# Optimization experiments

Measured on AMD Instinct MI355X. Metric: run time of the kernel, lower is better.

## Reference

```python
import jax, jax.numpy as jnp
import numpy as np

B, S, E = 8, 2048, 1024

def setup_inputs() -> dict:
    key = jax.random.key(0)
    ks = jax.random.split(key, 7)
    scale = 1.0 / np.sqrt(E)
    return {
        "x": jax.random.normal(ks[0], (B, S, E), dtype=jnp.float32),
        "Wq": jax.random.normal(ks[1], (E, E), dtype=jnp.float32) * scale,
        "bq": jax.random.normal(ks[2], (E,), dtype=jnp.float32) * 0.01,
        "Wk": jax.random.normal(ks[3], (E, E), dtype=jnp.float32) * scale,
        "bk": jax.random.normal(ks[4], (E,), dtype=jnp.float32) * 0.01,
        "Wv": jax.random.normal(ks[5], (E, E), dtype=jnp.float32) * scale,
        "bv": jax.random.normal(ks[6], (E,), dtype=jnp.float32) * 0.01,
    }

def reference(x, Wq, bq, Wk, bk, Wv, bv):
    # torch Linear: y = x @ W^T + b
    q = jnp.einsum('bse,fe->bsf', x, Wq) + bq  # [B,S,E]
    k = jnp.einsum('bse,fe->bsf', x, Wk) + bk
    v = jnp.einsum('bse,fe->bsf', x, Wv) + bv
    # unscaled, unmasked single-head attention (faithful to source)
    scores = jnp.einsum('bqe,bke->bqk', q, k)  # [B,S,S]
    attn = jax.nn.softmax(scores, axis=-1)
    return jnp.einsum('bqk,bke->bqe', attn, v)  # [B,S,E]
```

## Files before the change

kernel.cpp:

```cpp
#include <hip/hip_runtime.h>
#include <math.h>

typedef _Float16 f16;
typedef _Float16 f16x8 __attribute__((ext_vector_type(8)));
typedef _Float16 f16x4 __attribute__((ext_vector_type(4)));
typedef float f32x4v __attribute__((ext_vector_type(4)));

#define Bb 8
#define Ss 2048
#define Ee 1024
#define BSr (Bb*Ss)
#define MB 1048576ull

__device__ __forceinline__ void gll16(const void* gp, void* lp) {
    __builtin_amdgcn_global_load_lds(
        (const __attribute__((address_space(1))) unsigned int*)gp,
        (__attribute__((address_space(3))) unsigned int*)lp,
        16, 0, 0);
}

#define MFMA16(a, b, c) __builtin_amdgcn_mfma_f32_16x16x32_f16((a), (b), (c), 0, 0, 0)
#define SBAR() asm volatile("s_barrier" ::: "memory")

__global__ __launch_bounds__(256)
void split_xw(const float* __restrict__ x, const float* __restrict__ Wv,
              f16* __restrict__ xh, f16* __restrict__ Wvh)
{
    const int bid = blockIdx.x;
    const float* src; f16* dst; int i;
    if (bid < 16384) { src = x;  dst = xh;  i = (bid * 256 + threadIdx.x) * 4; }
    else             { src = Wv; dst = Wvh; i = ((bid - 16384) * 256 + threadIdx.x) * 4; }
    float4 v = *(const float4*)&src[i];
    f16x4 h4;
    h4[0] = (f16)v.x; h4[1] = (f16)v.y; h4[2] = (f16)v.z; h4[3] = (f16)v.w;
    *(f16x4*)&dst[i] = h4;
}

__global__ __launch_bounds__(256)
void transpose_split(const float* __restrict__ Wq, const float* __restrict__ Wk,
                     f16* __restrict__ WqTh, f16* __restrict__ WqTl,
                     f16* __restrict__ WkTh, f16* __restrict__ WkTl)
{
    __shared__ float ts[64][65];
    const int z = blockIdx.z;
    const float* W = z ? Wk : Wq;
    f16* Th = z ? WkTh : WqTh;
    f16* Tl = z ? WkTl : WqTl;
    const int e0 = blockIdx.x * 64, j0 = blockIdx.y * 64;
    const int t = threadIdx.x;
    {
        const int jj = t >> 2, c0 = (t & 3) * 16;
        #pragma unroll
        for (int m = 0; m < 4; ++m) {
            float4 v = *(const float4*)&W[(size_t)(j0 + jj) * Ee + e0 + c0 + m * 4];
            ts[jj][c0 + m*4 + 0] = v.x; ts[jj][c0 + m*4 + 1] = v.y;
            ts[jj][c0 + m*4 + 2] = v.z; ts[jj][c0 + m*4 + 3] = v.w;
        }
    }
    __syncthreads();
    {
        const int ee = t >> 2, jc0 = (t & 3) * 16;
        f16x8 h0, h1, l0, l1;
        #pragma unroll
        for (int m = 0; m < 16; ++m) {
            float val = ts[jc0 + m][ee];
            f16 hh = (f16)val; f16 ll = (f16)(val - (float)hh);
            if (m < 8) { h0[m] = hh; l0[m] = ll; }
            else       { h1[m-8] = hh; l1[m-8] = ll; }
        }
        size_t off = (size_t)(e0 + ee) * Ee + j0 + jc0;
        *(f16x8*)&Th[off]     = h0; *(f16x8*)&Th[off + 8] = h1;
        *(f16x8*)&Tl[off]     = l0; *(f16x8*)&Tl[off + 8] = l1;
    }
}

__global__ __launch_bounds__(256)
void compute_Mt(const f16* __restrict__ WkTh, const f16* __restrict__ WkTl,
                const f16* __restrict__ WqTh, const f16* __restrict__ WqTl,
                float* __restrict__ Mpart)
{
    __shared__ f16 Ah[128][32];
    __shared__ f16 Al[128][32];
    __shared__ f16 Bh[128][32];
    __shared__ f16 Bl[128][32];

    const int bn = blockIdx.x, bm = blockIdx.y, z = blockIdx.z;
    const int t = threadIdx.x;
    const int lane = t & 63;
    const int w = t >> 6;
    const int wr = w >> 1, wc = w & 1;
    const int lr = lane & 15;
    const int kq = (lane >> 4) << 3;
    const int rS = w * 32 + (lane >> 2);
    const int eS = (lane & 3) * 8;

    const f16* gAh = WkTh + ((size_t)(bm * 128 + rS)) * Ee + z * 256 + eS;
    const f16* gAl = WkTl + ((size_t)(bm * 128 + rS)) * Ee + z * 256 + eS;
    const f16* gBh = WqTh + ((size_t)(bn * 128 + rS)) * Ee + z * 256 + eS;
    const f16* gBl = WqTl + ((size_t)(bn * 128 + rS)) * Ee + z * 256 + eS;

    f32x4v acc[4][4];
    #pragma unroll
    for (int i = 0; i < 4; ++i)
        #pragma unroll
        for (int j = 0; j < 4; ++j) acc[i][j] = (f32x4v)0.f;

    for (int k0 = 0; k0 < 256; k0 += 32) {
        __syncthreads();
        #pragma unroll
        for (int c = 0; c < 2; ++c) {
            const size_t go = (size_t)c * 16 * Ee + k0;
            const int lo = w * 1024 + c * 512;
            gll16(gAh + go, &Ah[0][0] + lo);
            gll16(gAl + go, &Al[0][0] + lo);
            gll16(gBh + go, &Bh[0][0] + lo);
            gll16(gBl + go, &Bl[0][0] + lo);
        }
        __syncthreads();

        f16x8 fah[4], fal[4], fbh[4], fbl[4];
        #pragma unroll
        for (int i = 0; i < 4; ++i) {
            fah[i] = *(const f16x8*)&Ah[wr * 64 + i * 16 + lr][kq];
            fal[i] = *(const f16x8*)&Al[wr * 64 + i * 16 + lr][kq];
            fbh[i] = *(const f16x8*)&Bh[wc * 64 + i * 16 + lr][kq];
            fbl[i] = *(const f16x8*)&Bl[wc * 64 + i * 16 + lr][kq];
        }
        #pragma unroll
        for (int i = 0; i < 4; ++i)
            #pragma unroll
            for (int j = 0; j < 4; ++j) {
                acc[i][j] = MFMA16(fah[i], fbh[j], acc[i][j]);
                acc[i][j] = MFMA16(fah[i], fbl[j], acc[i][j]);
                acc[i][j] = MFMA16(fal[i], fbh[j], acc[i][j]);
            }
    }

    #pragma unroll
    for (int i = 0; i < 4; ++i) {
        #pragma unroll
        for (int j = 0; j < 4; ++j) {
            const int col = bn * 128 + wc * 64 + j * 16 + lr;
            #pragma unroll
            for (int r = 0; r < 4; ++r) {
                const int row = bm * 128 + wr * 64 + i * 16 + (lane >> 4) * 4 + r;
                Mpart[(size_t)z * MB + (size_t)row * Ee + col] = acc[i][j][r];
            }
        }
    }
}

__global__ __launch_bounds__(256)
void reduce_Mt(const float* __restrict__ Mpart, f16* __restrict__ Mth, f16* __restrict__ Mtl)
{
    const size_t i4 = ((size_t)blockIdx.x * 256 + threadIdx.x) * 4;
    float4 a = *(const float4*)&Mpart[i4];
    float4 b = *(const float4*)&Mpart[MB + i4];
    float4 c = *(const float4*)&Mpart[2 * MB + i4];
    float4 d = *(const float4*)&Mpart[3 * MB + i4];
    float s[4] = {a.x + b.x + c.x + d.x, a.y + b.y + c.y + d.y,
                  a.z + b.z + c.z + d.z, a.w + b.w + c.w + d.w};
    f16x4 h, l;
    #pragma unroll
    for (int m = 0; m < 4; ++m) { f16 hh = (f16)s[m]; h[m] = hh; l[m] = (f16)(s[m] - (float)hh); }
    *(f16x4*)&Mth[i4] = h;
    *(f16x4*)&Mtl[i4] = l;
}

__global__ __launch_bounds__(256)
void wker(const float* __restrict__ Wk, const float* __restrict__ bq,
          float* __restrict__ wpart)
{
    const int f = (blockIdx.x & 3) * 256 + threadIdx.x;
    const int p = blockIdx.x >> 2;
    float acc = 0.f;
    for (int j = p * 128; j < p * 128 + 128; ++j)
        acc += Wk[(size_t)j * Ee + f] * bq[j];
    wpart[p * Ee + f] = acc;
}

__global__ __launch_bounds__(256)
void vker(const f16* __restrict__ xh, const float* __restrict__ wpart,
          float* __restrict__ vbuf)
{
    __shared__ float wsum[1024];
    const int t = threadIdx.x;
    for (int ff = t; ff < 1024; ff += 256) {
        float s = 0.f;
        #pragma unroll
        for (int p = 0; p < 8; ++p) s += wpart[p * Ee + ff];
        wsum[ff] = s;
    }
    __syncthreads();
    const int lane = t & 63;
    const int row = blockIdx.x * 4 + (t >> 6);
    const f16* xr = xh + (size_t)row * Ee + lane * 16;
    f16x8 a = *(const f16x8*)&xr[0];
    f16x8 b = *(const f16x8*)&xr[8];
    float acc = 0.f;
    #pragma unroll
    for (int m = 0; m < 8; ++m) {
        acc += (float)a[m] * wsum[lane * 16 + m];
        acc += (float)b[m] * wsum[lane * 16 + 8 + m];
    }
    #pragma unroll
    for (int off = 1; off < 64; off <<= 1) acc += __shfl_xor(acc, off, 64);
    if (lane == 0) vbuf[row] = acc;
}

template<bool DUAL>
__device__ __forceinline__ void kloop32(
    const f16* __restrict__ Ag, const int sA,
    const f16* __restrict__ Bhg, const f16* __restrict__ Blg, const int sB,
    const int NT, f16* __restrict__ lds,
    f32x4v acc[8][4], const int w, const int lane)
{
    constexpr int SETF = DUAL ? 24576 : 16384;
    const int wr = w >> 2, wc = w & 3;
    const int srcA = (w * 16 + (lane & 15)) * sA + (lane >> 4) * 8;
    const int srcB = (w * 16 + (lane & 15)) * sB + (lane >> 4) * 8;
    const int lrd = lane * 8;

#define STAGE8(t, s) do {                                                   \
        const int k0_ = (t) * 32;                                           \
        const f16* gA_ = Ag + k0_ + srcA;                                   \
        const f16* gB_ = Bhg + k0_ + srcB;                                  \
        f16* dA_ = lds + (s) * SETF + w * 512;                              \
        f16* dB_ = lds + (s) * SETF + 8192 + w * 512;                       \
        gll16(gA_,                       dA_);                              \
        gll16(gA_ + (size_t)8 * 16 * sA, dA_ + 8 * 512);                    \
        gll16(gB_,                       dB_);                              \
        gll16(gB_ + (size_t)8 * 16 * sB, dB_ + 8 * 512);                    \
        if (DUAL) {                                                         \
            const f16* gL_ = Blg + k0_ + srcB;                              \
            f16* dL_ = lds + (s) * SETF + 16384 + w * 512;                  \
            gll16(gL_,                       dL_);                          \
            gll16(gL_ + (size_t)8 * 16 * sB, dL_ + 8 * 512);                \
        }                                                                   \
    } while (0)

    STAGE8(0, 0);
    STAGE8(1, 1);
    if (DUAL) asm volatile("s_waitcnt vmcnt(6)" ::: "memory");
    else      asm volatile("s_waitcnt vmcnt(4)" ::: "memory");
    SBAR();

    for (int t = 0; t < NT; ++t) {
        const int s = t % 3;
        if (t + 2 < NT) STAGE8(t + 2, (t + 2) % 3);

        const f16* As = lds + s * SETF;
        const f16* Bh = As + 8192;
        const f16* Bl = As + 16384;
        f16x8 fa[8], fbh[4], fbl[4];
        #pragma unroll
        for (int i = 0; i < 8; ++i)
            fa[i] = *(const f16x8*)(As + (wr * 8 + i) * 512 + lrd);
        #pragma unroll
        for (int j = 0; j < 4; ++j)
            fbh[j] = *(const f16x8*)(Bh + (wc * 4 + j) * 512 + lrd);
        if (DUAL) {
            #pragma unroll
            for (int j = 0; j < 4; ++j)
                fbl[j] = *(const f16x8*)(Bl + (wc * 4 + j) * 512 + lrd);
        }
        #pragma unroll
        for (int j = 0; j < 4; ++j)
            #pragma unroll
            for (int i = 0; i < 8; ++i) {
                acc[i][j] = MFMA16(fa[i], fbh[j], acc[i][j]);
                if (DUAL)
                    acc[i][j] = MFMA16(fa[i], fbl[j], acc[i][j]);
            }

        if (t + 2 < NT) {
            if (DUAL) asm volatile("s_waitcnt vmcnt(6)" ::: "memory");
            else      asm volatile("s_waitcnt vmcnt(4)" ::: "memory");
        } else if (t + 1 < NT) {
            asm volatile("s_waitcnt vmcnt(0)" ::: "memory");
        }
        SBAR();
    }
#undef STAGE8
}

__global__ __launch_bounds__(512, 2)
void proj3(const f16* __restrict__ xh,
           const f16* __restrict__ Mth, const f16* __restrict__ Mtl,
           const f16* __restrict__ Wvh, const float* __restrict__ bv,
           f16* __restrict__ qp, f16* __restrict__ vT)
{
    __shared__ f16 lds[73728];

    const int lin = blockIdx.x;
    const int l = (lin & 7) * 64 + (lin >> 3);
    const int zc = l & 7;
    const int by = l >> 3;
    const int z = zc >> 2;
    const int col0 = (zc & 3) * 256;
    const int row0 = by * 256;

    const int t = threadIdx.x;
    const int lane = t & 63;
    const int w = t >> 6;
    const int wr = w >> 2, wc = w & 3;

    f32x4v acc[8][4];
    #pragma unroll
    for (int i = 0; i < 8; ++i)
        #pragma unroll
        for (int j = 0; j < 4; ++j) acc[i][j] = (f32x4v)0.f;

    const f16* Ax = xh + (size_t)row0 * Ee;
    if (z == 0) {
        kloop32<true>(Ax, Ee, Mth + (size_t)col0 * Ee, Mtl + (size_t)col0 * Ee, Ee,
                      32, lds, acc, w, lane);
        #pragma unroll
        for (int i = 0; i < 8; ++i) {
            #pragma unroll
            for (int j = 0; j < 4; ++j) {
                const int col = col0 + wc * 64 + j * 16 + (lane & 15);
                #pragma unroll
                for (int r = 0; r < 4; ++r) {
                    const int row = row0 + wr * 128 + i * 16 + (lane >> 4) * 4 + r;
                    qp[(size_t)row * Ee + col] = (f16)acc[i][j][r];
                }
            }
        }
    } else {
        kloop32<false>(Ax, Ee, Wvh + (size_t)col0 * Ee, Wvh + (size_t)col0 * Ee, Ee,
                       32, lds, acc, w, lane);
        #pragma unroll
        for (int i = 0; i < 8; ++i) {
            #pragma unroll
            for (int j = 0; j < 4; ++j) {
                const int e = col0 + wc * 64 + j * 16 + (lane & 15);
                const float b = bv[e];
                const int srow = row0 + wr * 128 + i * 16 + (lane >> 4) * 4;
                const int bb = srow >> 11;
                const int s = srow & 2047;
                f16x4 pk;
                #pragma unroll
                for (int r = 0; r < 4; ++r) pk[r] = (f16)(acc[i][j][r] + b);
                *(f16x4*)&vT[((size_t)bb * Ee + e) * Ss + s] = pk;
            }
        }
    }
}

__global__ __launch_bounds__(512, 2)
void score8(const f16* __restrict__ qp, const f16* __restrict__ xh,
            const float* __restrict__ vbuf, float* __restrict__ Sbuf, int batch0)
{
    __shared__ f16 lds[49152];

    const int lin = blockIdx.x;
    const int cpx = gridDim.x >> 3;
    const int l = (lin & 7) * cpx + (lin >> 3);
    const int bn = l & 7;
    const int bm = (l >> 3) & 7;
    const int zb = l >> 6;
    const int b = batch0 + zb;

    const int t = threadIdx.x;
    const int lane = t & 63;
    const int w = t >> 6;
    const int wr = w >> 2, wc = w & 3;

    const f16* Aq = qp + ((size_t)b * Ss + bm * 256) * Ee;
    const f16* Bk = xh + ((size_t)b * Ss + bn * 256) * Ee;

    f32x4v acc[8][4];
    #pragma unroll
    for (int i = 0; i < 8; ++i)
        #pragma unroll
        for (int j = 0; j < 4; ++j) acc[i][j] = (f32x4v)0.f;

    kloop32<false>(Aq, Ee, Bk, Bk, Ee, 32, lds, acc, w, lane);

    #pragma unroll
    for (int i = 0; i < 8; ++i) {
        #pragma unroll
        for (int j = 0; j < 4; ++j) {
            const int col = bn * 256 + wc * 64 + j * 16 + (lane & 15);
            const float vv = vbuf[(size_t)b * Ss + col];
            #pragma unroll
            for (int r = 0; r < 4; ++r) {
                const int row = zb * Ss + bm * 256 + wr * 128 + i * 16 + (lane >> 4) * 4 + r;
                Sbuf[(size_t)row * 2048 + col] = acc[i][j][r] + vv;
            }
        }
    }
}

__global__ __launch_bounds__(256)
void softmax_rows(float* __restrict__ Sbuf)
{
    __shared__ float red[8];
    const int t = threadIdx.x;
    const int w = t >> 6;
    float* Srow = Sbuf + (size_t)blockIdx.x * 2048;

    float4 a = *(const float4*)&Srow[t * 8];
    float4 c = *(const float4*)&Srow[t * 8 + 4];
    float v[8] = {a.x, a.y, a.z, a.w, c.x, c.y, c.z, c.w};

    float m = v[0];
    #pragma unroll
    for (int i = 1; i < 8; ++i) m = fmaxf(m, v[i]);
    #pragma unroll
    for (int off = 1; off < 64; off <<= 1) m = fmaxf(m, __shfl_xor(m, off, 64));
    if ((t & 63) == 0) red[w] = m;
    __syncthreads();
    m = fmaxf(fmaxf(red[0], red[1]), fmaxf(red[2], red[3]));

    float e[8], s = 0.f;
    #pragma unroll
    for (int i = 0; i < 8; ++i) { e[i] = __expf(v[i] - m); s += e[i]; }
    #pragma unroll
    for (int off = 1; off < 64; off <<= 1) s += __shfl_xor(s, off, 64);
    if ((t & 63) == 0) red[4 + w] = s;
    __syncthreads();
    s = red[4] + red[5] + red[6] + red[7];

    const float inv = 1.0f / s;
    f16x8 pk;
    #pragma unroll
    for (int i = 0; i < 8; ++i) pk[i] = (f16)(e[i] * inv);
    *(f16x8*)(((f16*)Srow) + t * 8) = pk;
}

__global__ __launch_bounds__(512, 2)
void pv256(const float* __restrict__ Sbuf, const f16* __restrict__ vT,
           float* __restrict__ out)
{
    __shared__ f16 lds[49152];

    const int lin = blockIdx.x;
    const int l = (lin & 7) * 32 + (lin >> 3);
    const int bn = l & 3;
    const int bm = (l >> 2) & 7;
    const int b  = l >> 5;

    const int t = threadIdx.x;
    const int lane = t & 63;
    const int w = t >> 6;
    const int wr = w >> 2, wc = w & 3;

    const f16* gA = (const f16*)Sbuf + ((size_t)(b * Ss + bm * 256)) * 4096;
    const f16* gB = vT + ((size_t)b * Ee + bn * 256) * Ss;

    f32x4v acc[8][4];
    #pragma unroll
    for (int i = 0; i < 8; ++i)
        #pragma unroll
        for (int j = 0; j < 4; ++j) acc[i][j] = (f32x4v)0.f;

    kloop32<false>(gA, 4096, gB, gB, Ss, 64, lds, acc, w, lane);

    #pragma unroll
    for (int i = 0; i < 8; ++i) {
        #pragma unroll
        for (int j = 0; j < 4; ++j) {
            const int col = bn * 256 + wc * 64 + j * 16 + (lane & 15);
            #pragma unroll
            for (int r = 0; r < 4; ++r) {
                const int row = bm * 256 + wr * 128 + i * 16 + (lane >> 4) * 4 + r;
                out[((size_t)b * Ss + row) * Ee + col] = acc[i][j][r];
            }
        }
    }
}

__global__ __launch_bounds__(256)
void pv_gemm(const float* __restrict__ Sbuf, const f16* __restrict__ vT,
             float* __restrict__ out, int batch0)
{
    __shared__ f16 Pt[128][32];
    __shared__ f16 Vt[128][32];

    const int zb = blockIdx.z;
    const int b = batch0 + zb;
    const int bm = blockIdx.y;
    const int bn = blockIdx.x;

    const int t = threadIdx.x;
    const int lane = t & 63;
    const int w = t >> 6;
    const int wr = w >> 1, wc = w & 1;
    const int lr = lane & 15;
    const int kq = (lane >> 4) << 3;

    const int rS = w * 32 + (lane >> 2);
    const int eS = (lane & 3) * 8;

    const f16* Pbase = (const f16*)Sbuf;
    const f16* gA = Pbase + ((size_t)(zb * Ss + bm * 128 + rS)) * 4096 + eS;
    const f16* gB = vT + ((size_t)b * Ee + bn * 128 + rS) * Ss + eS;

    f32x4v acc[4][4];
    #pragma unroll
    for (int i = 0; i < 4; ++i)
        #pragma unroll
        for (int j = 0; j < 4; ++j) acc[i][j] = (f32x4v)0.f;

    for (int k0 = 0; k0 < Ss; k0 += 32) {
        __syncthreads();
        #pragma unroll
        for (int c = 0; c < 2; ++c) {
            const int lo = w * 1024 + c * 512;
            gll16(gA + (size_t)c * 16 * 4096 + k0, &Pt[0][0] + lo);
            gll16(gB + (size_t)c * 16 * Ss + k0,   &Vt[0][0] + lo);
        }
        __syncthreads();

        f16x8 fa[4], fb[4];
        #pragma unroll
        for (int i = 0; i < 4; ++i) {
            fa[i] = *(const f16x8*)&Pt[wr * 64 + i * 16 + lr][kq];
            fb[i] = *(const f16x8*)&Vt[wc * 64 + i * 16 + lr][kq];
        }
        #pragma unroll
        for (int i = 0; i < 4; ++i)
            #pragma unroll
            for (int j = 0; j < 4; ++j)
                acc[i][j] = MFMA16(fa[i], fb[j], acc[i][j]);
    }

    #pragma unroll
    for (int i = 0; i < 4; ++i) {
        #pragma unroll
        for (int j = 0; j < 4; ++j) {
            const int col = bn * 128 + wc * 64 + j * 16 + lr;
            #pragma unroll
            for (int r = 0; r < 4; ++r) {
                const int row = bm * 128 + wr * 64 + i * 16 + (lane >> 4) * 4 + r;
                out[((size_t)b * Ss + row) * Ee + col] = acc[i][j][r];
            }
        }
    }
}

#define TQ 16
#define TK 256
#define EC 64
#define NCH (Ee/EC)
#define NT  (Ss/TK)

__global__ __launch_bounds__(256)
void qkv_gemm(const float* __restrict__ x,
              const float* __restrict__ Wq, const float* __restrict__ bq,
              const float* __restrict__ Wk, const float* __restrict__ bk,
              const float* __restrict__ Wv, const float* __restrict__ bv,
              float* __restrict__ oq, float* __restrict__ ok, float* __restrict__ ov)
{
    __shared__ float Xs[64][17];
    __shared__ float Ws[64][17];
    const int t = threadIdx.x;
    const int z = blockIdx.z;
    const float* __restrict__ W    = (z == 0) ? Wq : ((z == 1) ? Wk : Wv);
    const float* __restrict__ bias = (z == 0) ? bq : ((z == 1) ? bk : bv);
    float* __restrict__ out        = (z == 0) ? oq : ((z == 1) ? ok : ov);

    const int row0 = blockIdx.y << 6;
    const int col0 = blockIdx.x << 6;
    const int ti = t >> 4;
    const int tj = t & 15;
    const int lr = t >> 2;
    const int lc = (t & 3) << 2;

    float acc[4][4];
    #pragma unroll
    for (int i = 0; i < 4; ++i)
        #pragma unroll
        for (int j = 0; j < 4; ++j) acc[i][j] = 0.f;

    for (int e0 = 0; e0 < Ee; e0 += 16) {
        __syncthreads();
        {
            float4 xv = *(const float4*)&x[(row0 + lr)*Ee + e0 + lc];
            float4 wv = *(const float4*)&W[(col0 + lr)*Ee + e0 + lc];
            Xs[lr][lc]   = xv.x; Xs[lr][lc+1] = xv.y; Xs[lr][lc+2] = xv.z; Xs[lr][lc+3] = xv.w;
            Ws[lr][lc]   = wv.x; Ws[lr][lc+1] = wv.y; Ws[lr][lc+2] = wv.z; Ws[lr][lc+3] = wv.w;
        }
        __syncthreads();
        #pragma unroll
        for (int ee = 0; ee < 16; ++ee) {
            float xa[4], wb[4];
            #pragma unroll
            for (int i = 0; i < 4; ++i) xa[i] = Xs[(ti<<2)+i][ee];
            #pragma unroll
            for (int j = 0; j < 4; ++j) wb[j] = Ws[(tj<<2)+j][ee];
            #pragma unroll
            for (int i = 0; i < 4; ++i)
                #pragma unroll
                for (int j = 0; j < 4; ++j)
                    acc[i][j] = fmaf(xa[i], wb[j], acc[i][j]);
        }
    }

    const float4 b4 = *(const float4*)&bias[col0 + (tj<<2)];
    #pragma unroll
    for (int i = 0; i < 4; ++i) {
        float4 o;
        o.x = acc[i][0] + b4.x;
        o.y = acc[i][1] + b4.y;
        o.z = acc[i][2] + b4.z;
        o.w = acc[i][3] + b4.w;
        *(float4*)&out[(row0 + (ti<<2) + i)*Ee + col0 + (tj<<2)] = o;
    }
}

__global__ __launch_bounds__(256)
void flash_attn(const float* __restrict__ qsrc,
                const float* __restrict__ ksrc,
                const float* __restrict__ vsrc,
                float* __restrict__ out)
{
    __shared__ float qs[TQ][1028];
    __shared__ float kv[TK][68];
    __shared__ float ps[TQ][260];
    __shared__ float f_s[TQ];
    __shared__ float l_s[TQ];

    const int t = threadIdx.x;
    const int lane = t & 63;
    const int w = t >> 6;
    const int q0 = blockIdx.x * TQ;
    const int kb = (q0 / Ss) * Ss;

    {
        const int r = t >> 4;
        const int c0 = (t & 15) << 2;
        #pragma unroll
        for (int m = 0; m < 16; ++m) {
            float4 v4 = *(const float4*)&qsrc[(q0 + r)*Ee + c0 + (m << 6)];
            *(float4*)&qs[r][c0 + (m << 6)] = v4;
        }
    }

    float4 oacc[NCH];
    #pragma unroll
    for (int i = 0; i < NCH; ++i) oacc[i] = make_float4(0.f, 0.f, 0.f, 0.f);
    float m_reg[4], l_reg[4];
    #pragma unroll
    for (int i = 0; i < 4; ++i) { m_reg[i] = -INFINITY; l_reg[i] = 0.f; }

    const int ow = t >> 4;
    const int oc = (t & 15) << 2;

    for (int kt = 0; kt < NT; ++kt) {
        const int kr0 = kb + kt * TK;

        float sacc[4][4];
        #pragma unroll
        for (int i = 0; i < 4; ++i)
            #pragma unroll
            for (int j = 0; j < 4; ++j) sacc[i][j] = 0.f;

        for (int ec = 0; ec < NCH; ++ec) {
            __syncthreads();
            {
                const int rr = t >> 4;
                const int cc = (t & 15) << 2;
                #pragma unroll
                for (int m = 0; m < 16; ++m) {
                    float4 v4 = *(const float4*)&ksrc[(kr0 + rr + (m<<4))*Ee + ec*EC + cc];
                    *(float4*)&kv[rr + (m<<4)][cc] = v4;
                }
            }
            __syncthreads();
            #pragma unroll 4
            for (int ee = 0; ee < EC; ee += 4) {
                float4 q4[4];
                #pragma unroll
                for (int i = 0; i < 4; ++i)
                    q4[i] = *(const float4*)&qs[(w<<2)+i][ec*EC + ee];
                #pragma unroll
                for (int j = 0; j < 4; ++j) {
                    float4 k4 = *(const float4*)&kv[lane + (j<<6)][ee];
                    #pragma unroll
                    for (int i = 0; i < 4; ++i) {
                        sacc[i][j] = fmaf(q4[i].x, k4.x, sacc[i][j]);
                        sacc[i][j] = fmaf(q4[i].y, k4.y, sacc[i][j]);
                        sacc[i][j] = fmaf(q4[i].z, k4.z, sacc[i][j]);
                        sacc[i][j] = fmaf(q4[i].w, k4.w, sacc[i][j]);
                    }
                }
            }
        }

        float tmax[4];
        #pragma unroll
        for (int i = 0; i < 4; ++i)
            tmax[i] = fmaxf(fmaxf(sacc[i][0], sacc[i][1]), fmaxf(sacc[i][2], sacc[i][3]));
        #pragma unroll
        for (int off = 1; off < 64; off <<= 1) {
            #pragma unroll
            for (int i = 0; i < 4; ++i)
                tmax[i] = fmaxf(tmax[i], __shfl_xor(tmax[i], off, 64));
        }
        float rs[4], fi[4];
        #pragma unroll
        for (int i = 0; i < 4; ++i) {
            float mn = fmaxf(m_reg[i], tmax[i]);
            fi[i] = __expf(m_reg[i] - mn);
            m_reg[i] = mn;
            float r = 0.f;
            #pragma unroll
            for (int j = 0; j < 4; ++j) {
                float p = __expf(sacc[i][j] - mn);
                ps[(w<<2)+i][lane + (j<<6)] = p;
                r += p;
            }
            rs[i] = r;
        }
        #pragma unroll
        for (int off = 1; off < 64; off <<= 1) {
            #pragma unroll
            for (int i = 0; i < 4; ++i)
                rs[i] += __shfl_xor(rs[i], off, 64);
        }
        #pragma unroll
        for (int i = 0; i < 4; ++i)
            l_reg[i] = l_reg[i] * fi[i] + rs[i];
        if (lane == 0) {
            #pragma unroll
            for (int i = 0; i < 4; ++i) {
                f_s[(w<<2)+i] = fi[i];
                l_s[(w<<2)+i] = l_reg[i];
            }
        }
        __syncthreads();

        const float fown = f_s[ow];
        #pragma unroll
        for (int c4 = 0; c4 < NCH; ++c4) {
            oacc[c4].x *= fown; oacc[c4].y *= fown;
            oacc[c4].z *= fown; oacc[c4].w *= fown;
        }
        for (int pc = 0; pc < NCH; ++pc) {
            __syncthreads();
            {
                const int rr = t >> 4;
                const int cc = (t & 15) << 2;
                #pragma unroll
                for (int m = 0; m < 16; ++m) {
                    float4 v4 = *(const float4*)&vsrc[(kr0 + rr + (m<<4))*Ee + pc*EC + cc];
                    *(float4*)&kv[rr + (m<<4)][cc] = v4;
                }
            }
            __syncthreads();
            float4 acc = oacc[pc];
            #pragma unroll 4
            for (int tj0 = 0; tj0 < TK; tj0 += 4) {
                float4 p4 = *(const float4*)&ps[ow][tj0];
                float4 v0 = *(const float4*)&kv[tj0+0][oc];
                float4 v1 = *(const float4*)&kv[tj0+1][oc];
                float4 v2 = *(const float4*)&kv[tj0+2][oc];
                float4 v3 = *(const float4*)&kv[tj0+3][oc];
                acc.x = fmaf(p4.x, v0.x, acc.x); acc.y = fmaf(p4.x, v0.y, acc.y);
                acc.z = fmaf(p4.x, v0.z, acc.z); acc.w = fmaf(p4.x, v0.w, acc.w);
                acc.x = fmaf(p4.y, v1.x, acc.x); acc.y = fmaf(p4.y, v1.y, acc.y);
                acc.z = fmaf(p4.y, v1.z, acc.z); acc.w = fmaf(p4.y, v1.w, acc.w);
                acc.x = fmaf(p4.z, v2.x, acc.x); acc.y = fmaf(p4.z, v2.y, acc.y);
                acc.z = fmaf(p4.z, v2.z, acc.z); acc.w = fmaf(p4.z, v2.w, acc.w);
                acc.x = fmaf(p4.w, v3.x, acc.x); acc.y = fmaf(p4.w, v3.y, acc.y);
                acc.z = fmaf(p4.w, v3.z, acc.z); acc.w = fmaf(p4.w, v3.w, acc.w);
            }
            oacc[pc] = acc;
        }
    }

    __syncthreads();
    const float linv = 1.0f / l_s[ow];
    #pragma unroll
    for (int c4 = 0; c4 < NCH; ++c4) {
        float4 o = oacc[c4];
        o.x *= linv; o.y *= linv; o.z *= linv; o.w *= linv;
        *(float4*)&out[(q0 + ow)*Ee + oc + (c4 << 6)] = o;
    }
}

extern "C" void kernel_launch(void* const* d_in, const int* in_sizes, int n_in,
                              void* d_out, int out_size, void* d_ws, size_t ws_size,
                              hipStream_t stream)
{
    (void)in_sizes; (void)n_in; (void)out_size;
    const float* x  = (const float*)d_in[0];
    const float* Wq = (const float*)d_in[1];
    const float* bq = (const float*)d_in[2];
    const float* Wk = (const float*)d_in[3];
    const float* bk = (const float*)d_in[4];  (void)bk;
    const float* Wv = (const float*)d_in[5];
    const float* bv = (const float*)d_in[6];
    float* out = (float*)d_out;

    const size_t S8 = 128 * MB, S4 = 64 * MB, S2 = 32 * MB;
    const size_t TAIL = 96 * MB + 16 * MB + MB;
    const size_t NEED8 = S8 + TAIL;
    const size_t NEED4 = S4 + TAIL;
    const size_t NEED2 = S2 + TAIL;

    if (ws_size >= NEED2) {
        const int nb = (ws_size >= NEED8) ? 8 : ((ws_size >= NEED4) ? 4 : 2);
        const size_t sb = (nb == 8) ? S8 : ((nb == 4) ? S4 : S2);
        char* base = (char*)d_ws;
        float* Sbuf = (float*)base;
        f16* xh   = (f16*)(base + sb);
        f16* qp   = (f16*)(base + sb + 32 * MB);
        f16* vT   = (f16*)(base + sb + 64 * MB);
        f16* Wvh  = (f16*)(base + sb + 96 * MB);
        f16* WqTh = (f16*)(base + sb + 98 * MB);
        f16* WqTl = (f16*)(base + sb + 100 * MB);
        f16* WkTh = (f16*)(base + sb + 102 * MB);
        f16* WkTl = (f16*)(base + sb + 104 * MB);
        f16* Mth  = (f16*)(base + sb + 106 * MB);
        f16* Mtl  = (f16*)(base + sb + 108 * MB);
        float* Mpart = (float*)(base + sb + 110 * MB);
        float* wpart = (float*)(base + sb + 126 * MB);
        float* vbuf  = (float*)(base + sb + 126 * MB + 65536);

        split_xw<<<17408, 256, 0, stream>>>(x, Wv, xh, Wvh);
        transpose_split<<<dim3(16, 16, 2), 256, 0, stream>>>(Wq, Wk, WqTh, WqTl, WkTh, WkTl);
        compute_Mt<<<dim3(8, 8, 4), 256, 0, stream>>>(WkTh, WkTl, WqTh, WqTl, Mpart);
        reduce_Mt<<<1024, 256, 0, stream>>>(Mpart, Mth, Mtl);
        wker<<<32, 256, 0, stream>>>(Wk, bq, wpart);
        vker<<<4096, 256, 0, stream>>>(xh, wpart, vbuf);
        proj3<<<512, 512, 0, stream>>>(xh, Mth, Mtl, Wvh, bv, qp, vT);
        if (nb == 8) {
            score8<<<512, 512, 0, stream>>>(qp, xh, vbuf, Sbuf, 0);
            softmax_rows<<<16384, 256, 0, stream>>>(Sbuf);
            pv256<<<256, 512, 0, stream>>>(Sbuf, vT, out);
        } else {
            for (int c = 0; c < 8 / nb; ++c) {
                score8<<<64 * nb, 512, 0, stream>>>(qp, xh, vbuf, Sbuf, nb * c);
                softmax_rows<<<nb * 2048, 256, 0, stream>>>(Sbuf);
                pv_gemm<<<dim3(8, 16, nb), 256, 0, stream>>>(Sbuf, vT, out, nb * c);
            }
        }
    } else {
        float* kbuf = (float*)d_ws;
        float* vbuf2 = kbuf + (size_t)BSr * Ee;
        dim3 g1(Ee / 64, BSr / 64, 3);
        qkv_gemm<<<g1, 256, 0, stream>>>(x, Wq, bq, Wk, bk, Wv, bv, out, kbuf, vbuf2);
        flash_attn<<<dim3(BSr / TQ), 256, 0, stream>>>(out, kbuf, vbuf2, out);
    }
}
```

Before: 362.9 us.

## Double-buffer LDS fragment reads in GEMM k-loop and relax launch bounds

The k-loop is unrolled by two, with two register sets for the A/B fragments, so the LDS reads for the next tile are issued before the MFMAs of the current tile run. Scheduling barriers keep the compiler from reordering them. Launch bounds on the three GEMM kernels drop from 2 to 1 block per CU, which frees registers for the doubled fragment sets at the cost of occupancy. The wait before each barrier is now a full vmcnt(0), so the global prefetch gets less time to overlap.

```diff
diff --git a/kernel.cpp b/kernel.cpp
--- a/kernel.cpp
+++ b/kernel.cpp
@@ -220,6 +220,9 @@
     const int srcA = (w * 16 + (lane & 15)) * sA + (lane >> 4) * 8;
     const int srcB = (w * 16 + (lane & 15)) * sB + (lane >> 4) * 8;
     const int lrd = lane * 8;
+
+    f16x8 fa0[8], fbh0[4], fbl0[4];
+    f16x8 fa1[8], fbh1[4], fbl1[4];
 
 #define STAGE8(t, s) do {                                                   \
         const int k0_ = (t) * 32;                                           \
@@ -239,52 +242,66 @@
         }                                                                   \
     } while (0)
 
+#define READF(t, FA, FBH, FBL) do {                                         \
+        const f16* As_ = lds + ((t) % 3) * SETF;                            \
+        const f16* Bh_ = As_ + 8192;                                        \
+        const f16* Bl_ = As_ + 16384;                                       \
+        _Pragma("unroll")                                                   \
+        for (int i_ = 0; i_ < 8; ++i_)                                      \
+            FA[i_] = *(const f16x8*)(As_ + (wr * 8 + i_) * 512 + lrd);      \
+        _Pragma("unroll")                                                   \
+        for (int j_ = 0; j_ < 4; ++j_)                                      \
+            FBH[j_] = *(const f16x8*)(Bh_ + (wc * 4 + j_) * 512 + lrd);     \
+        if (DUAL) {                                                         \
+            _Pragma("unroll")                                               \
+            for (int j_ = 0; j_ < 4; ++j_)                                  \
+                FBL[j_] = *(const f16x8*)(Bl_ + (wc * 4 + j_) * 512 + lrd); \
+        }                                                                   \
+    } while (0)
+
+#define MFMAS(FA, FBH, FBL) do {                                            \
+        _Pragma("unroll")                                                   \
+        for (int j_ = 0; j_ < 4; ++j_)                                      \
+            _Pragma("unroll")                                               \
+            for (int i_ = 0; i_ < 8; ++i_) {                                \
+                acc[i_][j_] = MFMA16(FA[i_], FBH[j_], acc[i_][j_]);         \
+                if (DUAL)                                                   \
+                    acc[i_][j_] = MFMA16(FA[i_], FBL[j_], acc[i_][j_]);     \
+            }                                                               \
+    } while (0)
+
     STAGE8(0, 0);
     STAGE8(1, 1);
-    if (DUAL) asm volatile("s_waitcnt vmcnt(6)" ::: "memory");
-    else      asm volatile("s_waitcnt vmcnt(4)" ::: "memory");
+    asm volatile("s_waitcnt vmcnt(0)" ::: "memory");
     SBAR();
-
-    for (int t = 0; t < NT; ++t) {
-        const int s = t % 3;
+    READF(0, fa0, fbh0, fbl0);
+
+    for (int t = 0; t < NT; t += 2) {
+        if (t + 1 < NT) READF(t + 1, fa1, fbh1, fbl1);
         if (t + 2 < NT) STAGE8(t + 2, (t + 2) % 3);
-
-        const f16* As = lds + s * SETF;
-        const f16* Bh = As + 8192;
-        const f16* Bl = As + 16384;
-        f16x8 fa[8], fbh[4], fbl[4];
-        #pragma unroll
-        for (int i = 0; i < 8; ++i)
-            fa[i] = *(const f16x8*)(As + (wr * 8 + i) * 512 + lrd);
-        #pragma unroll
-        for (int j = 0; j < 4; ++j)
-            fbh[j] = *(const f16x8*)(Bh + (wc * 4 + j) * 512 + lrd);
-        if (DUAL) {
-            #pragma unroll
-            for (int j = 0; j < 4; ++j)
-                fbl[j] = *(const f16x8*)(Bl + (wc * 4 + j) * 512 + lrd);
-        }
-        #pragma unroll
-        for (int j = 0; j < 4; ++j)
-            #pragma unroll
-            for (int i = 0; i < 8; ++i) {
-                acc[i][j] = MFMA16(fa[i], fbh[j], acc[i][j]);
-                if (DUAL)
-                    acc[i][j] = MFMA16(fa[i], fbl[j], acc[i][j]);
-            }
-
-        if (t + 2 < NT) {
-            if (DUAL) asm volatile("s_waitcnt vmcnt(6)" ::: "memory");
-            else      asm volatile("s_waitcnt vmcnt(4)" ::: "memory");
-        } else if (t + 1 < NT) {
+        __builtin_amdgcn_sched_barrier(0);
+        MFMAS(fa0, fbh0, fbl0);
+        if (t + 1 < NT) {
             asm volatile("s_waitcnt vmcnt(0)" ::: "memory");
-        }
-        SBAR();
+            SBAR();
+        }
+        if (t + 1 < NT) {
+            if (t + 2 < NT) READF(t + 2, fa0, fbh0, fbl0);
+            if (t + 3 < NT) STAGE8(t + 3, (t + 3) % 3);
+            __builtin_amdgcn_sched_barrier(0);
+            MFMAS(fa1, fbh1, fbl1);
+            if (t + 2 < NT) {
+                asm volatile("s_waitcnt vmcnt(0)" ::: "memory");
+                SBAR();
+            }
+        }
     }
 #undef STAGE8
-}
-
-__global__ __launch_bounds__(512, 2)
+#undef READF
+#undef MFMAS
+}
+
+__global__ __launch_bounds__(512, 1)
 void proj3(const f16* __restrict__ xh,
            const f16* __restrict__ Mth, const f16* __restrict__ Mtl,
            const f16* __restrict__ Wvh, const float* __restrict__ bv,
@@ -348,7 +365,7 @@
     }
 }
 
-__global__ __launch_bounds__(512, 2)
+__global__ __launch_bounds__(512, 1)
 void score8(const f16* __restrict__ qp, const f16* __restrict__ xh,
             const float* __restrict__ vbuf, float* __restrict__ Sbuf, int batch0)
 {
@@ -430,7 +447,7 @@
     *(f16x8*)(((f16*)Srow) + t * 8) = pk;
 }
 
-__global__ __launch_bounds__(512, 2)
+__global__ __launch_bounds__(512, 1)
 void pv256(const float* __restrict__ Sbuf, const f16* __restrict__ vT,
            float* __restrict__ out)
 {
```

Measured after the change: 530.5 us. 1.46x slower.
